# Kernel tuning notes

Hardware: AMD Instinct MI355X
Metric: run time of the kernel (lower is better)

Reference implementation:

```python
import jax, jax.numpy as jnp
import numpy as np

BASIS_ORDER = 7  # basis_dim = 8 (Chebyshev T_0..T_7 of tanh(x))


def chebyshev_basis(x, order=BASIS_ORDER):
    """x: [batch, in] -> [batch, in, order+1] Chebyshev basis on tanh(x)."""
    xt = jnp.tanh(x)
    terms = [jnp.ones_like(xt), xt]
    for _ in range(2, order + 1):
        terms.append(2.0 * xt * terms[-1] - terms[-2])
    return jnp.stack(terms[: order + 1], axis=-1)


def setup_inputs() -> dict:
    key = jax.random.key(0)
    k1, k2, k3 = jax.random.split(key, 3)
    batch, in_f, out_f, K = 4096, 1024, 1024, BASIS_ORDER + 1
    x = jax.random.normal(k1, (batch, in_f), dtype=jnp.float32)
    # Kaiming-uniform-ish init scale
    bound = 1.0 / np.sqrt(in_f * K)
    weights = jax.random.uniform(k2, (out_f, in_f, K), dtype=jnp.float32,
                                 minval=-bound, maxval=bound)
    bias_param = jax.random.uniform(k3, (out_f,), dtype=jnp.float32,
                                    minval=-bound, maxval=bound)
    return {"x": x, "weights": weights, "bias_param": bias_param}


def reference(x, weights, bias_param):
    # basis: [b, i, k]; weights: [o, i, k] -> out[b, o] = sum_{i,k} basis*W
    basis = chebyshev_basis(x)  # [batch, in, K]
    out = jnp.einsum('bik,oik->bo', basis, weights)
    return out + bias_param
```

## Files before the change

### kernel.cpp

```cpp
#include <hip/hip_runtime.h>
#include <hip/hip_bf16.h>

#define MD 4096
#define ND 1024
#define KD 8192
#define IN_F 1024

typedef __bf16 bf16x8 __attribute__((ext_vector_type(8)));
typedef float f32x4 __attribute__((ext_vector_type(4)));

#define N_BASIS (MD * IN_F)
#define N_CONV ((ND * KD) / 8)

__global__ __launch_bounds__(256) void prep_kernel(
    const float* __restrict__ x, const float* __restrict__ w,
    __bf16* __restrict__ A, __bf16* __restrict__ B) {
  int i = blockIdx.x * blockDim.x + threadIdx.x;
  if (i < N_BASIS) {
    float t = tanhf(x[i]);
    float two_t = 2.0f * t;
    float T0 = 1.0f;
    float T1 = t;
    float T2 = two_t * T1 - T0;
    float T3 = two_t * T2 - T1;
    float T4 = two_t * T3 - T2;
    float T5 = two_t * T4 - T3;
    float T6 = two_t * T5 - T4;
    float T7 = two_t * T6 - T5;
    bf16x8 v;
    v[0] = (__bf16)T0; v[1] = (__bf16)T1; v[2] = (__bf16)T2; v[3] = (__bf16)T3;
    v[4] = (__bf16)T4; v[5] = (__bf16)T5; v[6] = (__bf16)T6; v[7] = (__bf16)T7;
    *(bf16x8*)(A + (size_t)i * 8) = v;
  } else if (i < N_BASIS + N_CONV) {
    int j = i - N_BASIS;
    const float4* p = (const float4*)(w + (size_t)j * 8);
    float4 a = p[0], b = p[1];
    bf16x8 v;
    v[0] = (__bf16)a.x; v[1] = (__bf16)a.y; v[2] = (__bf16)a.z; v[3] = (__bf16)a.w;
    v[4] = (__bf16)b.x; v[5] = (__bf16)b.y; v[6] = (__bf16)b.z; v[7] = (__bf16)b.w;
    *(bf16x8*)(B + (size_t)j * 8) = v;
  }
}

#define BM 128
#define BN 128
#define BK 64
#define NT (KD / BK)
#define TSZ (BM * BK)

__global__ __launch_bounds__(256, 1) void gemm_bias(
    const __bf16* __restrict__ A, const __bf16* __restrict__ B,
    const float* __restrict__ bias, float* __restrict__ C) {
  __shared__ __align__(16) __bf16 As[3][TSZ];
  __shared__ __align__(16) __bf16 Bs[3][TSZ];

  const int tid = threadIdx.x;
  const int wave = tid >> 6;
  const int lane = tid & 63;

  const int b = blockIdx.x;
  const int xcd = b & 7;
  const int j = b >> 3;
  const int nt = j & 7;
  const int mloc = j >> 3;
  const int n0 = nt * BN;
  const int m0 = (xcd * 4 + mloc) * BM;

  const int wm = wave >> 1;
  const int wn = wave & 1;

  const int ar = lane >> 3;
  const int swz_col = ((lane & 7) ^ ar) * 8;
  const __bf16* gA = A + (size_t)(m0 + wave * 32 + ar) * KD + swz_col;
  const __bf16* gB = B + (size_t)(n0 + wave * 32 + ar) * KD + swz_col;
  const int loff = wave * 32 * BK;

  f32x4 acc[4][4];
#pragma unroll
  for (int i = 0; i < 4; i++)
#pragma unroll
    for (int jj = 0; jj < 4; jj++) acc[i][jj] = (f32x4){0.f, 0.f, 0.f, 0.f};

  const int fr = lane & 15;
  const int fr7 = fr & 7;
  const int qk = lane >> 4;

#pragma unroll
  for (int jj = 0; jj < 4; jj++) {
    __builtin_amdgcn_global_load_lds(
        (const __attribute__((address_space(1))) void*)(gA + (size_t)jj * 8 * KD),
        (__attribute__((address_space(3))) void*)(&As[0][loff + jj * 8 * BK]), 16, 0, 0);
    __builtin_amdgcn_global_load_lds(
        (const __attribute__((address_space(1))) void*)(gB + (size_t)jj * 8 * KD),
        (__attribute__((address_space(3))) void*)(&Bs[0][loff + jj * 8 * BK]), 16, 0, 0);
  }

#define ITER(T, CUR, NXT, WAIT)                                                \
  do {                                                                         \
    const int tn = ((T) + 1 < NT) ? (T) + 1 : 0;                               \
    _Pragma("unroll") for (int jj = 0; jj < 4; jj++) {                         \
      __builtin_amdgcn_global_load_lds(                                        \
          (const __attribute__((address_space(1))) void*)(                     \
              gA + (size_t)tn * BK + (size_t)jj * 8 * KD),                     \
          (__attribute__((address_space(3))) void*)(                           \
              &As[NXT][loff + jj * 8 * BK]), 16, 0, 0);                        \
      __builtin_amdgcn_global_load_lds(                                        \
          (const __attribute__((address_space(1))) void*)(                     \
              gB + (size_t)tn * BK + (size_t)jj * 8 * KD),                     \
          (__attribute__((address_space(3))) void*)(                           \
              &Bs[NXT][loff + jj * 8 * BK]), 16, 0, 0);                        \
    }                                                                          \
    asm volatile(WAIT ::: "memory");                                           \
    __builtin_amdgcn_s_barrier();                                              \
    asm volatile("" ::: "memory");                                             \
    _Pragma("unroll") for (int s = 0; s < 2; s++) {                            \
      const int pa = ((s * 4 + qk) ^ fr7) * 8;                                 \
      bf16x8 af[4], bfr[4];                                                    \
      _Pragma("unroll") for (int mi = 0; mi < 4; mi++)                         \
          af[mi] = *(const bf16x8*)&As[CUR][(wm * 64 + mi * 16 + fr) * BK + pa]; \
      _Pragma("unroll") for (int ni = 0; ni < 4; ni++)                         \
          bfr[ni] = *(const bf16x8*)&Bs[CUR][(wn * 64 + ni * 16 + fr) * BK + pa]; \
      _Pragma("unroll") for (int mi = 0; mi < 4; mi++)                         \
          _Pragma("unroll") for (int ni = 0; ni < 4; ni++)                     \
              acc[mi][ni] = __builtin_amdgcn_mfma_f32_16x16x32_bf16(           \
                  af[mi], bfr[ni], acc[mi][ni], 0, 0, 0);                      \
    }                                                                          \
  } while (0)

  ITER(0, 0, 1, "s_waitcnt vmcnt(0)");
  ITER(1, 1, 2, "s_waitcnt vmcnt(8)");
  ITER(2, 2, 0, "s_waitcnt vmcnt(8)");
#pragma unroll 1
  for (int t0 = 3; t0 < 126; t0 += 3) {
    ITER(t0, 0, 1, "s_waitcnt vmcnt(8)");
    ITER(t0 + 1, 1, 2, "s_waitcnt vmcnt(8)");
    ITER(t0 + 2, 2, 0, "s_waitcnt vmcnt(8)");
  }
  ITER(126, 0, 1, "s_waitcnt vmcnt(8)");
  ITER(127, 1, 2, "s_waitcnt vmcnt(8)");
#undef ITER

  const int col0 = n0 + wn * 64;
  const int row0 = m0 + wm * 64 + qk * 4;
#pragma unroll
  for (int ni = 0; ni < 4; ni++) {
    int col = col0 + ni * 16 + fr;
    float bv = bias[col];
#pragma unroll
    for (int mi = 0; mi < 4; mi++) {
      int row = row0 + mi * 16;
#pragma unroll
      for (int r = 0; r < 4; r++)
        C[(size_t)(row + r) * ND + col] = acc[mi][ni][r] + bv;
    }
  }
}

extern "C" void kernel_launch(void* const* d_in, const int* in_sizes, int n_in,
                              void* d_out, int out_size, void* d_ws, size_t ws_size,
                              hipStream_t stream) {
  const float* x = (const float*)d_in[0];
  const float* w = (const float*)d_in[1];
  const float* bias = (const float*)d_in[2];
  float* out = (float*)d_out;

  __bf16* Abf = (__bf16*)d_ws;
  __bf16* Bbf = (__bf16*)((char*)d_ws + (size_t)MD * KD * 2);

  {
    int n = N_BASIS + N_CONV;
    prep_kernel<<<(n + 255) / 256, 256, 0, stream>>>(x, w, Abf, Bbf);
  }
  {
    gemm_bias<<<256, 256, 0, stream>>>(Abf, Bbf, bias, out);
  }
}
```

Baseline: 183.7 us.

## Load A operand directly from global into registers, bypassing LDS

The A tile is no longer staged through shared memory. Each wave now loads its own A MFMA fragments straight from global memory into registers, one K-tile ahead. Only B still goes through the triple-buffered LDS path, and the vmcnt thresholds are raised to cover the extra outstanding global loads. This cuts LDS traffic and LDS footprint for A. In exchange, waves sharing the same A rows fetch them twice from global/L2, the access pattern is less coalesced, and the register prefetch only looks one tile ahead.

```diff
diff --git a/kernel.cpp b/kernel.cpp
--- a/kernel.cpp
+++ b/kernel.cpp
@@ -46,12 +46,11 @@
 #define BN 128
 #define BK 64
 #define NT (KD / BK)
-#define TSZ (BM * BK)
+#define TSZ (BN * BK)
 
 __global__ __launch_bounds__(256, 1) void gemm_bias(
     const __bf16* __restrict__ A, const __bf16* __restrict__ B,
     const float* __restrict__ bias, float* __restrict__ C) {
-  __shared__ __align__(16) __bf16 As[3][TSZ];
   __shared__ __align__(16) __bf16 Bs[3][TSZ];
 
   const int tid = threadIdx.x;
@@ -71,9 +70,17 @@
 
   const int ar = lane >> 3;
   const int swz_col = ((lane & 7) ^ ar) * 8;
-  const __bf16* gA = A + (size_t)(m0 + wave * 32 + ar) * KD + swz_col;
   const __bf16* gB = B + (size_t)(n0 + wave * 32 + ar) * KD + swz_col;
   const int loff = wave * 32 * BK;
+
+  const int fr = lane & 15;
+  const int fr7 = fr & 7;
+  const int qk = lane >> 4;
+
+  const __bf16* ap[4];
+#pragma unroll
+  for (int mi = 0; mi < 4; mi++)
+    ap[mi] = A + (size_t)(m0 + wm * 64 + mi * 16 + fr) * KD + qk * 8;
 
   f32x4 acc[4][4];
 #pragma unroll
@@ -81,63 +88,60 @@
 #pragma unroll
     for (int jj = 0; jj < 4; jj++) acc[i][jj] = (f32x4){0.f, 0.f, 0.f, 0.f};
 
-  const int fr = lane & 15;
-  const int fr7 = fr & 7;
-  const int qk = lane >> 4;
-
 #pragma unroll
-  for (int jj = 0; jj < 4; jj++) {
-    __builtin_amdgcn_global_load_lds(
-        (const __attribute__((address_space(1))) void*)(gA + (size_t)jj * 8 * KD),
-        (__attribute__((address_space(3))) void*)(&As[0][loff + jj * 8 * BK]), 16, 0, 0);
+  for (int jj = 0; jj < 4; jj++)
     __builtin_amdgcn_global_load_lds(
         (const __attribute__((address_space(1))) void*)(gB + (size_t)jj * 8 * KD),
         (__attribute__((address_space(3))) void*)(&Bs[0][loff + jj * 8 * BK]), 16, 0, 0);
-  }
+  bf16x8 a_cur[4][2];
+#pragma unroll
+  for (int mi = 0; mi < 4; mi++)
+#pragma unroll
+    for (int s = 0; s < 2; s++)
+      a_cur[mi][s] = *(const bf16x8*)(ap[mi] + s * 32);
 
 #define ITER(T, CUR, NXT, WAIT)                                                \
   do {                                                                         \
     const int tn = ((T) + 1 < NT) ? (T) + 1 : 0;                               \
-    _Pragma("unroll") for (int jj = 0; jj < 4; jj++) {                         \
-      __builtin_amdgcn_global_load_lds(                                        \
-          (const __attribute__((address_space(1))) void*)(                     \
-              gA + (size_t)tn * BK + (size_t)jj * 8 * KD),                     \
-          (__attribute__((address_space(3))) void*)(                           \
-              &As[NXT][loff + jj * 8 * BK]), 16, 0, 0);                        \
-      __builtin_amdgcn_global_load_lds(                                        \
-          (const __attribute__((address_space(1))) void*)(                     \
-              gB + (size_t)tn * BK + (size_t)jj * 8 * KD),                     \
-          (__attribute__((address_space(3))) void*)(                           \
-              &Bs[NXT][loff + jj * 8 * BK]), 16, 0, 0);                        \
-    }                                                                          \
+    _Pragma("unroll") for (int jj = 0; jj < 4; jj++)                           \
+        __builtin_amdgcn_global_load_lds(                                      \
+            (const __attribute__((address_space(1))) void*)(                   \
+                gB + (size_t)tn * BK + (size_t)jj * 8 * KD),                   \
+            (__attribute__((address_space(3))) void*)(                         \
+                &Bs[NXT][loff + jj * 8 * BK]), 16, 0, 0);                      \
+    bf16x8 a_nxt[4][2];                                                        \
+    _Pragma("unroll") for (int mi = 0; mi < 4; mi++)                           \
+        _Pragma("unroll") for (int s = 0; s < 2; s++)                          \
+            a_nxt[mi][s] = *(const bf16x8*)(ap[mi] + tn * 64 + s * 32);        \
     asm volatile(WAIT ::: "memory");                                           \
     __builtin_amdgcn_s_barrier();                                              \
     asm volatile("" ::: "memory");                                             \
     _Pragma("unroll") for (int s = 0; s < 2; s++) {                            \
       const int pa = ((s * 4 + qk) ^ fr7) * 8;                                 \
-      bf16x8 af[4], bfr[4];                                                    \
-      _Pragma("unroll") for (int mi = 0; mi < 4; mi++)                         \
-          af[mi] = *(const bf16x8*)&As[CUR][(wm * 64 + mi * 16 + fr) * BK + pa]; \
+      bf16x8 bfr[4];                                                           \
       _Pragma("unroll") for (int ni = 0; ni < 4; ni++)                         \
           bfr[ni] = *(const bf16x8*)&Bs[CUR][(wn * 64 + ni * 16 + fr) * BK + pa]; \
       _Pragma("unroll") for (int mi = 0; mi < 4; mi++)                         \
           _Pragma("unroll") for (int ni = 0; ni < 4; ni++)                     \
               acc[mi][ni] = __builtin_amdgcn_mfma_f32_16x16x32_bf16(           \
-                  af[mi], bfr[ni], acc[mi][ni], 0, 0, 0);                      \
+                  a_cur[mi][s], bfr[ni], acc[mi][ni], 0, 0, 0);                \
     }                                                                          \
+    _Pragma("unroll") for (int mi = 0; mi < 4; mi++)                           \
+        _Pragma("unroll") for (int s = 0; s < 2; s++)                          \
+            a_cur[mi][s] = a_nxt[mi][s];                                       \
   } while (0)
 
   ITER(0, 0, 1, "s_waitcnt vmcnt(0)");
-  ITER(1, 1, 2, "s_waitcnt vmcnt(8)");
-  ITER(2, 2, 0, "s_waitcnt vmcnt(8)");
+  ITER(1, 1, 2, "s_waitcnt vmcnt(12)");
+  ITER(2, 2, 0, "s_waitcnt vmcnt(12)");
 #pragma unroll 1
   for (int t0 = 3; t0 < 126; t0 += 3) {
-    ITER(t0, 0, 1, "s_waitcnt vmcnt(8)");
-    ITER(t0 + 1, 1, 2, "s_waitcnt vmcnt(8)");
-    ITER(t0 + 2, 2, 0, "s_waitcnt vmcnt(8)");
+    ITER(t0, 0, 1, "s_waitcnt vmcnt(12)");
+    ITER(t0 + 1, 1, 2, "s_waitcnt vmcnt(12)");
+    ITER(t0 + 2, 2, 0, "s_waitcnt vmcnt(12)");
   }
-  ITER(126, 0, 1, "s_waitcnt vmcnt(8)");
-  ITER(127, 1, 2, "s_waitcnt vmcnt(8)");
+  ITER(126, 0, 1, "s_waitcnt vmcnt(12)");
+  ITER(127, 1, 2, "s_waitcnt vmcnt(12)");
 #undef ITER
 
   const int col0 = n0 + wn * 64;
```

After: 254.1 us. +38.3%, slower.
